# Kernel optimization log

Measured on AMD Instinct MI355X. Metric: run time of the kernel, lower is better.

The kernel has to match this reference:

```python
import jax, jax.numpy as jnp
import numpy as np

V, S, E, H, D, L = 32000, 1024, 512, 8, 64, 4
FF = 4 * E
EPS = 1e-5


def setup_inputs() -> dict:
    key = jax.random.key(0)
    ks = jax.random.split(key, 24)
    s = 0.02
    inp = {
        "x": jax.random.randint(ks[0], (2, S), 0, V, dtype=jnp.int32),
        "tok_emb": jax.random.normal(ks[1], (V, E), jnp.float32) * s,
        "pos_emb": jax.random.normal(ks[2], (S, E), jnp.float32) * s,
        "Wq": jax.random.normal(ks[3], (L, H, E, D), jnp.float32) * s,
        "bq": jnp.zeros((L, H, D), jnp.float32),
        "Wk": jax.random.normal(ks[4], (L, H, E, D), jnp.float32) * s,
        "bk": jnp.zeros((L, H, D), jnp.float32),
        "Wv": jax.random.normal(ks[5], (L, H, E, D), jnp.float32) * s,
        "bv": jnp.zeros((L, H, D), jnp.float32),
        "Wo": jax.random.normal(ks[6], (L, H * D, E), jnp.float32) * s,
        "bo": jnp.zeros((L, E), jnp.float32),
        "W1": jax.random.normal(ks[7], (L, E, FF), jnp.float32) * s,
        "b1": jnp.zeros((L, FF), jnp.float32),
        "W2": jax.random.normal(ks[8], (L, FF, E), jnp.float32) * s,
        "b2": jnp.zeros((L, E), jnp.float32),
        "ln1_g": jnp.ones((L, E), jnp.float32),
        "ln1_b": jnp.zeros((L, E), jnp.float32),
        "ln2_g": jnp.ones((L, E), jnp.float32),
        "ln2_b": jnp.zeros((L, E), jnp.float32),
        "Wout": jax.random.normal(ks[9], (E, V), jnp.float32) * s,
        "bout": jnp.zeros((V,), jnp.float32),
    }
    return inp


def _layernorm(x, g, b):
    mu = jnp.mean(x, axis=-1, keepdims=True)
    var = jnp.mean(jnp.square(x - mu), axis=-1, keepdims=True)
    return (x - mu) * jax.lax.rsqrt(var + EPS) * g + b


def _decoder(h, Wq, bq, Wk, bk, Wv, bv, Wo, bo, W1, b1, W2, b2, g1, be1, g2, be2):
    B, T, _ = h.shape
    # per-head Q/K/V projections, batched over heads (matches concat of per-head linears)
    Q = jnp.einsum("bse,hed->bhsd", h, Wq) + bq[None, :, None, :]
    K = jnp.einsum("bse,hed->bhsd", h, Wk) + bk[None, :, None, :]
    Vv = jnp.einsum("bse,hed->bhsd", h, Wv) + bv[None, :, None, :]
    scores = jnp.einsum("bhqd,bhkd->bhqk", Q, K) / jnp.sqrt(jnp.asarray(D, h.dtype))
    causal = jnp.tril(jnp.ones((T, T), bool))
    scores = jnp.where(causal[None, None], scores, -jnp.inf)
    attn = jax.nn.softmax(scores, axis=-1)
    out = jnp.einsum("bhqk,bhkd->bhqd", attn, Vv)
    conc = out.transpose(0, 2, 1, 3).reshape(B, T, H * D)  # concat heads along feature dim
    mha = conc @ Wo + bo
    ln = _layernorm(h + mha, g1, be1)
    ff = jax.nn.relu(ln @ W1 + b1) @ W2 + b2
    return _layernorm(ln + ff, g2, be2)


def reference(x, tok_emb, pos_emb, Wq, bq, Wk, bk, Wv, bv, Wo, bo,
              W1, b1, W2, b2, ln1_g, ln1_b, ln2_g, ln2_b, Wout, bout):
    B, T = x.shape
    h = tok_emb[x] + pos_emb[:T][None]  # [B,T,E]
    for l in range(L):
        h = _decoder(h, Wq[l], bq[l], Wk[l], bk[l], Wv[l], bv[l], Wo[l], bo[l],
                     W1[l], b1[l], W2[l], b2[l], ln1_g[l], ln1_b[l], ln2_g[l], ln2_b[l])
    return h @ Wout + bout  # [B,T,V] logits
```

## Files before the change

### kernel.cpp

```cpp
#include <hip/hip_runtime.h>
#include <hip/hip_bf16.h>


#define B_ 2
#define S_ 1024
#define E_ 512
#define H_ 8
#define D_ 64
#define L_ 4
#define FF_ 2048
#define V_ 32000
#define M_ (B_ * S_)
#define QKV_N (3 * H_ * D_)

typedef __attribute__((ext_vector_type(8))) short short8;
typedef __attribute__((ext_vector_type(4))) float f32x4;

__device__ __forceinline__ float b2f(ushort u) {
  union { uint32_t i; float f; } c; c.i = ((uint32_t)u) << 16; return c.f;
}
__device__ __forceinline__ ushort f2b(float f) {
  union { float f; uint32_t i; } c; c.f = f;
  uint32_t u = c.i;
  return (ushort)((u + 0x7FFFu + ((u >> 16) & 1u)) >> 16);
}

__device__ __forceinline__ void gload16(const ushort* g, ushort* l) {
  __builtin_amdgcn_global_load_lds(
      (const __attribute__((address_space(1))) void*)g,
      (__attribute__((address_space(3))) void*)l, 16, 0, 0);
}

__global__ __launch_bounds__(256) void embed_kernel(
    const int* __restrict__ x, const float* __restrict__ tok,
    const float* __restrict__ pos, float* __restrict__ hf,
    ushort* __restrict__ hb) {
  int idx = blockIdx.x * 256 + threadIdx.x;
  int e = idx & (E_ - 1);
  int t = (idx >> 9) & (S_ - 1);
  int b = idx >> 19;
  int tokid = x[b * S_ + t];
  float v = tok[(size_t)tokid * E_ + e] + pos[(size_t)t * E_ + e];
  hf[idx] = v;
  hb[idx] = f2b(v);
}

__global__ __launch_bounds__(256) void transpose_cvt_kernel(
    const float* __restrict__ in, ushort* __restrict__ out, int R, int C,
    int B2, long long inS1, long long inS2, long long outS1, long long outS2) {
  __shared__ float tile[32][33];
  int bz = blockIdx.z;
  int b1 = bz / B2, b2 = bz % B2;
  in += (size_t)b1 * inS1 + (size_t)b2 * inS2;
  out += (size_t)b1 * outS1 + (size_t)b2 * outS2;
  int r0 = blockIdx.x * 32, c0 = blockIdx.y * 32;
  int tx = threadIdx.x & 31, ty = threadIdx.x >> 5;
#pragma unroll
  for (int i = 0; i < 4; i++)
    tile[ty + 8 * i][tx] = in[(size_t)(r0 + ty + 8 * i) * C + c0 + tx];
  __syncthreads();
#pragma unroll
  for (int i = 0; i < 4; i++)
    out[(size_t)(c0 + ty + 8 * i) * R + r0 + tx] = f2b(tile[tx][ty + 8 * i]);
}

__global__ __launch_bounds__(256) void qkvw_kernel(
    const float* __restrict__ Wq, const float* __restrict__ Wk,
    const float* __restrict__ Wv, ushort* __restrict__ wqkv) {
  __shared__ float tile[32][33];
  int bz = blockIdx.z;
  int t = bz / (L_ * H_);
  int rem = bz % (L_ * H_);
  int lyr = rem / H_, h = rem % H_;
  const float* in = ((t == 0) ? Wq : (t == 1) ? Wk : Wv) +
                    ((size_t)lyr * H_ + h) * E_ * D_;
  ushort* out = wqkv + (size_t)lyr * QKV_N * E_ + ((size_t)t * 512 + h * 64) * E_;
  int r0 = blockIdx.x * 32, c0 = blockIdx.y * 32;
  int tx = threadIdx.x & 31, ty = threadIdx.x >> 5;
#pragma unroll
  for (int i = 0; i < 4; i++)
    tile[ty + 8 * i][tx] = in[(size_t)(r0 + ty + 8 * i) * D_ + c0 + tx];
  __syncthreads();
#pragma unroll
  for (int i = 0; i < 4; i++)
    out[(size_t)(c0 + ty + 8 * i) * E_ + r0 + tx] = f2b(tile[tx][ty + 8 * i]);
}

__global__ __launch_bounds__(256) void pack_b_kernel(
    const float* __restrict__ bq, const float* __restrict__ bk,
    const float* __restrict__ bv, float* __restrict__ bp) {
  int idx = blockIdx.x * 256 + threadIdx.x;
  if (idx >= L_ * QKV_N) return;
  int n = idx % QKV_N;
  int l = idx / QKV_N;
  int t = n / (H_ * D_);
  int hd = n % (H_ * D_);
  const float* src = (t == 0) ? bq : (t == 1) ? bk : bv;
  bp[idx] = src[(size_t)l * H_ * D_ + hd];
}

template <bool OUTBF, bool RELU, bool VT, bool SWZ>
__global__ __launch_bounds__(256) void mfma_gemm_kernel(
    const ushort* __restrict__ A, const ushort* __restrict__ Bt,
    const float* __restrict__ bias, const float* __restrict__ resid,
    void* __restrict__ out, ushort* __restrict__ vt,
    int M, int N, int K, int gx) {
  __shared__ __align__(16) ushort As[128 * 64];
  __shared__ __align__(16) ushort Bs[128 * 64];
  int tid = threadIdx.x;
  int w = tid >> 6, l = tid & 63;
  int wr = w >> 1, wc = w & 1;
  int lane15 = l & 15, lhi = l >> 4;

  int bid = blockIdx.x;
  int bx, by;
  if (SWZ) {
    int nwg = gx * (M >> 7);
    int wg = (bid & 7) * (nwg >> 3) + (bid >> 3);
    by = wg & ((M >> 7) - 1);
    bx = wg >> 4;
  } else {
    bx = bid % gx;
    by = bid / gx;
  }
  int row0 = by * 128, col0 = bx * 128;

  int rr8 = l >> 3;
  int ksrc = (((l & 7) ^ rr8) << 3);
  const ushort *gA[2][2], *gB[2][2];
  ushort *lA[2][2], *lB[2][2];
#pragma unroll
  for (int cc = 0; cc < 2; cc++) {
    int c = w + cc * 4;
#pragma unroll
    for (int h = 0; h < 2; h++) {
      int row = c * 16 + h * 8 + rr8;
      gA[cc][h] = A + (size_t)(row0 + row) * K + ksrc;
      gB[cc][h] = Bt + (size_t)(col0 + row) * K + ksrc;
      int ldst = c * 1024 + h * 512 + l * 8;
      lA[cc][h] = &As[ldst];
      lB[cc][h] = &Bs[ldst];
    }
  }

  f32x4 acc[4][4] = {};

  for (int k0 = 0; k0 < K; k0 += 64) {
#pragma unroll
    for (int cc = 0; cc < 2; cc++)
#pragma unroll
      for (int h = 0; h < 2; h++) {
        gload16(gA[cc][h] + k0, lA[cc][h]);
        gload16(gB[cc][h] + k0, lB[cc][h]);
      }
    __syncthreads();
    short8 a[4][2], b[4][2];
    int sa = (lane15 & 7) << 4;
#pragma unroll
    for (int i = 0; i < 4; i++) {
      int ra = (wr * 64 + i * 16 + lane15) * 64;
      int rb = (wc * 64 + i * 16 + lane15) * 64;
#pragma unroll
      for (int kk = 0; kk < 2; kk++) {
        int inner = ((kk * 64 + lhi * 16) ^ sa) >> 1;
        a[i][kk] = *(const short8*)&As[ra + inner];
        b[i][kk] = *(const short8*)&Bs[rb + inner];
      }
    }
#pragma unroll
    for (int i = 0; i < 4; i++)
#pragma unroll
      for (int j = 0; j < 4; j++) {
        acc[i][j] = __builtin_amdgcn_mfma_f32_16x16x32_bf16(a[i][0], b[j][0], acc[i][j], 0, 0, 0);
        acc[i][j] = __builtin_amdgcn_mfma_f32_16x16x32_bf16(a[i][1], b[j][1], acc[i][j], 0, 0, 0);
      }
    __syncthreads();
  }

  float* outf = (float*)out;
  ushort* outb = (ushort*)out;
#pragma unroll
  for (int i = 0; i < 4; i++) {
    int gr = row0 + wr * 64 + i * 16 + lhi * 4;
#pragma unroll
    for (int j = 0; j < 4; j++) {
      int gc = col0 + wc * 64 + j * 16 + lane15;
      float bb = bias[gc];
#pragma unroll
      for (int r = 0; r < 4; r++) {
        float v = acc[i][j][r] + bb;
        if (resid) v += resid[(size_t)(gr + r) * N + gc];
        if (RELU) v = fmaxf(v, 0.f);
        if (VT && gc >= 1024) {
          int d = gc - 1024;
          int grr = gr + r;
          int bb2 = grr >> 10, s = grr & 1023;
          vt[(((size_t)(bb2 * 8 + (d >> 6)) * 64 + (d & 63)) << 10) + s] = f2b(v);
        } else if (OUTBF) {
          outb[(size_t)(gr + r) * N + gc] = f2b(v);
        } else {
          outf[(size_t)(gr + r) * N + gc] = v;
        }
      }
    }
  }
}

template <int SK>
__global__ __launch_bounds__(256) void mfma_gemm_sk_kernel(
    const ushort* __restrict__ A, const ushort* __restrict__ Bt,
    float* __restrict__ part, int M, int N, int K, int gx) {
  __shared__ __align__(16) ushort As[128 * 64];
  __shared__ __align__(16) ushort Bs[128 * 64];
  int tid = threadIdx.x;
  int w = tid >> 6, l = tid & 63;
  int wr = w >> 1, wc = w & 1;
  int lane15 = l & 15, lhi = l >> 4;

  int tiles = gx * (M >> 7);
  int sk = blockIdx.x / tiles;
  int rem = blockIdx.x % tiles;
  int bx = rem % gx, by = rem / gx;
  int row0 = by * 128, col0 = bx * 128;
  int klen = K / SK, kbeg = sk * klen;

  int rr8 = l >> 3;
  int ksrc = (((l & 7) ^ rr8) << 3);
  const ushort *gA[2][2], *gB[2][2];
  ushort *lA[2][2], *lB[2][2];
#pragma unroll
  for (int cc = 0; cc < 2; cc++) {
    int c = w + cc * 4;
#pragma unroll
    for (int h = 0; h < 2; h++) {
      int row = c * 16 + h * 8 + rr8;
      gA[cc][h] = A + (size_t)(row0 + row) * K + ksrc;
      gB[cc][h] = Bt + (size_t)(col0 + row) * K + ksrc;
      int ldst = c * 1024 + h * 512 + l * 8;
      lA[cc][h] = &As[ldst];
      lB[cc][h] = &Bs[ldst];
    }
  }

  f32x4 acc[4][4] = {};

  for (int k0 = kbeg; k0 < kbeg + klen; k0 += 64) {
#pragma unroll
    for (int cc = 0; cc < 2; cc++)
#pragma unroll
      for (int h = 0; h < 2; h++) {
        gload16(gA[cc][h] + k0, lA[cc][h]);
        gload16(gB[cc][h] + k0, lB[cc][h]);
      }
    __syncthreads();
    short8 a[4][2], b[4][2];
    int sa = (lane15 & 7) << 4;
#pragma unroll
    for (int i = 0; i < 4; i++) {
      int ra = (wr * 64 + i * 16 + lane15) * 64;
      int rb = (wc * 64 + i * 16 + lane15) * 64;
#pragma unroll
      for (int kk = 0; kk < 2; kk++) {
        int inner = ((kk * 64 + lhi * 16) ^ sa) >> 1;
        a[i][kk] = *(const short8*)&As[ra + inner];
        b[i][kk] = *(const short8*)&Bs[rb + inner];
      }
    }
#pragma unroll
    for (int i = 0; i < 4; i++)
#pragma unroll
      for (int j = 0; j < 4; j++) {
        acc[i][j] = __builtin_amdgcn_mfma_f32_16x16x32_bf16(a[i][0], b[j][0], acc[i][j], 0, 0, 0);
        acc[i][j] = __builtin_amdgcn_mfma_f32_16x16x32_bf16(a[i][1], b[j][1], acc[i][j], 0, 0, 0);
      }
    __syncthreads();
  }

  float* dst = part + (size_t)sk * M * N;
#pragma unroll
  for (int i = 0; i < 4; i++) {
    int gr = row0 + wr * 64 + i * 16 + lhi * 4;
#pragma unroll
    for (int j = 0; j < 4; j++) {
      int gc = col0 + wc * 64 + j * 16 + lane15;
#pragma unroll
      for (int r = 0; r < 4; r++)
        dst[(size_t)(gr + r) * N + gc] = acc[i][j][r];
    }
  }
}

__global__ __launch_bounds__(128) void fattn_kernel(
    const ushort* __restrict__ qkv, const ushort* __restrict__ vt,
    ushort* __restrict__ conc) {
  int qb = blockIdx.x;
  int bh = blockIdx.y;
  int b = bh >> 3, h = bh & 7;
  int w = threadIdx.x >> 6, l = threadIdx.x & 63;
  int lane15 = l & 15, lhi = l >> 4;
  int q0 = qb * 32 + w * 16;

  __shared__ __align__(16) ushort plds[2][16][72];

  const ushort* qr = qkv + (size_t)(b * S_ + q0 + lane15) * QKV_N + h * 64;
  short8 qf0 = *(const short8*)(qr + lhi * 8);
  short8 qf1 = *(const short8*)(qr + 32 + lhi * 8);

  f32x4 o[4] = {};
  float m[4], lsum[4];
#pragma unroll
  for (int r = 0; r < 4; r++) { m[r] = -1e30f; lsum[r] = 0.f; }

  const ushort* kbase = qkv + (size_t)b * S_ * QKV_N + 512 + h * 64;
  const ushort* vbase = vt + (size_t)bh * 64 * S_;
  int qtop = q0 + 15;

  for (int kv0 = 0; kv0 <= qtop; kv0 += 64) {
    float sv[4][4];
#pragma unroll
    for (int t = 0; t < 4; t++) {
      if (kv0 + t * 16 <= qtop) {
        const ushort* kr = kbase + (size_t)(kv0 + t * 16 + lane15) * QKV_N;
        short8 kf0 = *(const short8*)(kr + lhi * 8);
        short8 kf1 = *(const short8*)(kr + 32 + lhi * 8);
        f32x4 s = {};
        s = __builtin_amdgcn_mfma_f32_16x16x32_bf16(qf0, kf0, s, 0, 0, 0);
        s = __builtin_amdgcn_mfma_f32_16x16x32_bf16(qf1, kf1, s, 0, 0, 0);
        int kidx = kv0 + t * 16 + lane15;
#pragma unroll
        for (int r = 0; r < 4; r++) {
          float v = s[r] * 0.125f;
          if (kidx > q0 + lhi * 4 + r) v = -1e30f;
          sv[t][r] = v;
        }
      } else {
#pragma unroll
        for (int r = 0; r < 4; r++) sv[t][r] = -1e30f;
      }
    }
#pragma unroll
    for (int r = 0; r < 4; r++) {
      float rm = fmaxf(fmaxf(sv[0][r], sv[1][r]), fmaxf(sv[2][r], sv[3][r]));
      rm = fmaxf(rm, __shfl_xor(rm, 1));
      rm = fmaxf(rm, __shfl_xor(rm, 2));
      rm = fmaxf(rm, __shfl_xor(rm, 4));
      rm = fmaxf(rm, __shfl_xor(rm, 8));
      float mn = fmaxf(m[r], rm);
      float sc = __expf(m[r] - mn);
      m[r] = mn;
      float rs = 0.f;
#pragma unroll
      for (int t = 0; t < 4; t++) {
        float p = __expf(sv[t][r] - mn);
        plds[w][lhi * 4 + r][t * 16 + lane15] = f2b(p);
        rs += p;
      }
      rs += __shfl_xor(rs, 1);
      rs += __shfl_xor(rs, 2);
      rs += __shfl_xor(rs, 4);
      rs += __shfl_xor(rs, 8);
      lsum[r] = lsum[r] * sc + rs;
#pragma unroll
      for (int n = 0; n < 4; n++) o[n][r] *= sc;
    }
    short8 pa0 = *(const short8*)&plds[w][lane15][lhi * 8];
    short8 pa1 = *(const short8*)&plds[w][lane15][32 + lhi * 8];
#pragma unroll
    for (int n = 0; n < 4; n++) {
      const ushort* vr = vbase + (size_t)(n * 16 + lane15) * S_ + kv0;
      short8 vf0 = *(const short8*)(vr + lhi * 8);
      short8 vf1 = *(const short8*)(vr + 32 + lhi * 8);
      o[n] = __builtin_amdgcn_mfma_f32_16x16x32_bf16(pa0, vf0, o[n], 0, 0, 0);
      o[n] = __builtin_amdgcn_mfma_f32_16x16x32_bf16(pa1, vf1, o[n], 0, 0, 0);
    }
  }
#pragma unroll
  for (int r = 0; r < 4; r++) {
    float inv = 1.f / lsum[r];
    int row = b * S_ + q0 + lhi * 4 + r;
#pragma unroll
    for (int n = 0; n < 4; n++)
      conc[(size_t)row * (H_ * D_) + h * 64 + n * 16 + lane15] = f2b(o[n][r] * inv);
  }
}

template <int SK>
__global__ __launch_bounds__(256) void ln_red_kernel(
    const float* __restrict__ part, const float* __restrict__ bias,
    const float* __restrict__ resid, const float* __restrict__ g,
    const float* __restrict__ bsh, float* __restrict__ outf,
    ushort* __restrict__ outb) {
  int w = threadIdx.x >> 6, l = threadIdx.x & 63;
  int row = blockIdx.x * 4 + w;
  size_t off = (size_t)row * E_ + l * 8;
  float4 r0 = *(const float4*)(resid + off);
  float4 r1 = *(const float4*)(resid + off + 4);
  float4 bb0 = *(const float4*)(bias + l * 8);
  float4 bb1 = *(const float4*)(bias + l * 8 + 4);
  float x[8] = {r0.x + bb0.x, r0.y + bb0.y, r0.z + bb0.z, r0.w + bb0.w,
                r1.x + bb1.x, r1.y + bb1.y, r1.z + bb1.z, r1.w + bb1.w};
#pragma unroll
  for (int s = 0; s < SK; s++) {
    const float* ps = part + (size_t)s * M_ * E_ + off;
    float4 p0 = *(const float4*)ps;
    float4 p1 = *(const float4*)(ps + 4);
    x[0] += p0.x; x[1] += p0.y; x[2] += p0.z; x[3] += p0.w;
    x[4] += p1.x; x[5] += p1.y; x[6] += p1.z; x[7] += p1.w;
  }
  float s = 0.f, q = 0.f;
#pragma unroll
  for (int i = 0; i < 8; i++) { s += x[i]; q += x[i] * x[i]; }
#pragma unroll
  for (int off2 = 1; off2 < 64; off2 <<= 1) {
    s += __shfl_xor(s, off2);
    q += __shfl_xor(q, off2);
  }
  float mu = s * (1.f / 512.f);
  float var = q * (1.f / 512.f) - mu * mu;
  float rs = rsqrtf(var + 1e-5f);
  float4 g0 = *(const float4*)(g + l * 8);
  float4 g1 = *(const float4*)(g + l * 8 + 4);
  float4 b0 = *(const float4*)(bsh + l * 8);
  float4 b1 = *(const float4*)(bsh + l * 8 + 4);
  float gg[8] = {g0.x, g0.y, g0.z, g0.w, g1.x, g1.y, g1.z, g1.w};
  float bbv[8] = {b0.x, b0.y, b0.z, b0.w, b1.x, b1.y, b1.z, b1.w};
  float y[8];
#pragma unroll
  for (int i = 0; i < 8; i++) y[i] = (x[i] - mu) * rs * gg[i] + bbv[i];
  float* of = outf + off;
  *(float4*)of = make_float4(y[0], y[1], y[2], y[3]);
  *(float4*)(of + 4) = make_float4(y[4], y[5], y[6], y[7]);
  ushort4 u0 = {f2b(y[0]), f2b(y[1]), f2b(y[2]), f2b(y[3])};
  ushort4 u1 = {f2b(y[4]), f2b(y[5]), f2b(y[6]), f2b(y[7])};
  ushort* ob = outb + off;
  *(ushort4*)ob = u0;
  *(ushort4*)(ob + 4) = u1;
}

extern "C" void kernel_launch(void* const* d_in, const int* in_sizes, int n_in,
                              void* d_out, int out_size, void* d_ws, size_t ws_size,
                              hipStream_t stream) {
  const int* x = (const int*)d_in[0];
  const float* tok = (const float*)d_in[1];
  const float* pos = (const float*)d_in[2];
  const float* Wq = (const float*)d_in[3];
  const float* bq = (const float*)d_in[4];
  const float* Wk = (const float*)d_in[5];
  const float* bk = (const float*)d_in[6];
  const float* Wv = (const float*)d_in[7];
  const float* bv = (const float*)d_in[8];
  const float* Wo = (const float*)d_in[9];
  const float* bo = (const float*)d_in[10];
  const float* W1 = (const float*)d_in[11];
  const float* b1 = (const float*)d_in[12];
  const float* W2 = (const float*)d_in[13];
  const float* b2 = (const float*)d_in[14];
  const float* ln1g = (const float*)d_in[15];
  const float* ln1b = (const float*)d_in[16];
  const float* ln2g = (const float*)d_in[17];
  const float* ln2b = (const float*)d_in[18];
  const float* Wout = (const float*)d_in[19];
  const float* bout = (const float*)d_in[20];
  float* out = (float*)d_out;

  char* p = (char*)d_ws;
  auto alloc = [&](size_t bytes) {
    char* r = p;
    p += (bytes + 255) & ~(size_t)255;
    return r;
  };
  float* h_f = (float*)alloc((size_t)M_ * E_ * 4);
  ushort* h_b = (ushort*)alloc((size_t)M_ * E_ * 2);
  ushort* qkv_b = (ushort*)alloc((size_t)M_ * QKV_N * 2);
  ushort* conc_b = (ushort*)alloc((size_t)M_ * E_ * 2);
  float* part = (float*)alloc((size_t)4 * M_ * E_ * 4);
  float* ln_f = (float*)alloc((size_t)M_ * E_ * 4);
  ushort* ln_b = (ushort*)alloc((size_t)M_ * E_ * 2);
  ushort* ff_b = (ushort*)alloc((size_t)M_ * FF_ * 2);
  ushort* vt_b = (ushort*)alloc((size_t)B_ * H_ * D_ * S_ * 2);
  ushort* wqkv = (ushort*)alloc((size_t)L_ * QKV_N * E_ * 2);
  float* bqkv = (float*)alloc((size_t)L_ * QKV_N * 4);
  ushort* wo_t = (ushort*)alloc((size_t)L_ * E_ * E_ * 2);
  ushort* w1_t = (ushort*)alloc((size_t)L_ * FF_ * E_ * 2);
  ushort* w2_t = (ushort*)alloc((size_t)L_ * E_ * FF_ * 2);
  ushort* wout_t = (ushort*)alloc((size_t)V_ * E_ * 2);

  qkvw_kernel<<<dim3(E_ / 32, D_ / 32, 3 * L_ * H_), 256, 0, stream>>>(Wq, Wk, Wv, wqkv);
  transpose_cvt_kernel<<<dim3(16, 16, L_), 256, 0, stream>>>(
      Wo, wo_t, 512, 512, 1, (long long)512 * 512, 0, (long long)512 * 512, 0);
  transpose_cvt_kernel<<<dim3(E_ / 32, FF_ / 32, L_), 256, 0, stream>>>(
      W1, w1_t, E_, FF_, 1, (long long)E_ * FF_, 0, (long long)FF_ * E_, 0);
  transpose_cvt_kernel<<<dim3(FF_ / 32, E_ / 32, L_), 256, 0, stream>>>(
      W2, w2_t, FF_, E_, 1, (long long)FF_ * E_, 0, (long long)E_ * FF_, 0);
  transpose_cvt_kernel<<<dim3(E_ / 32, V_ / 32, 1), 256, 0, stream>>>(
      Wout, wout_t, E_, V_, 1, 0, 0, 0, 0);
  pack_b_kernel<<<(L_ * QKV_N + 255) / 256, 256, 0, stream>>>(bq, bk, bv, bqkv);

  embed_kernel<<<(M_ * E_) / 256, 256, 0, stream>>>(x, tok, pos, h_f, h_b);

  for (int l = 0; l < L_; ++l) {
    mfma_gemm_kernel<true, false, true, false><<<(QKV_N / 128) * (M_ / 128), 256, 0, stream>>>(
        h_b, wqkv + (size_t)l * QKV_N * E_, bqkv + l * QKV_N, nullptr,
        qkv_b, vt_b, M_, QKV_N, E_, QKV_N / 128);
    fattn_kernel<<<dim3(S_ / 32, B_ * H_), 128, 0, stream>>>(qkv_b, vt_b, conc_b);
    mfma_gemm_sk_kernel<4><<<4 * (E_ / 128) * (M_ / 128), 256, 0, stream>>>(
        conc_b, wo_t + (size_t)l * E_ * E_, part, M_, E_, E_, E_ / 128);
    ln_red_kernel<4><<<M_ / 4, 256, 0, stream>>>(
        part, bo + l * E_, h_f, ln1g + l * E_, ln1b + l * E_, ln_f, ln_b);
    mfma_gemm_kernel<true, true, false, false><<<(FF_ / 128) * (M_ / 128), 256, 0, stream>>>(
        ln_b, w1_t + (size_t)l * FF_ * E_, b1 + l * FF_, nullptr, ff_b, nullptr,
        M_, FF_, E_, FF_ / 128);
    mfma_gemm_sk_kernel<4><<<4 * (E_ / 128) * (M_ / 128), 256, 0, stream>>>(
        ff_b, w2_t + (size_t)l * E_ * FF_, part, M_, E_, FF_, E_ / 128);
    ln_red_kernel<4><<<M_ / 4, 256, 0, stream>>>(
        part, b2 + l * E_, ln_f, ln2g + l * E_, ln2b + l * E_, h_f, h_b);
  }

  mfma_gemm_kernel<false, false, false, true><<<(V_ / 128) * (M_ / 128), 256, 0, stream>>>(
      h_b, wout_t, bout, nullptr, out, nullptr, M_, V_, E_, V_ / 128);
}
```

Baseline: 660.2 us.

## Use 256x256-tile double-buffered GEMM kernel for output vocab projection

Replaces the 128x128 swizzled GEMM for the final logits projection with a new 512-thread kernel that computes 256x256 output tiles and double-buffers its LDS stages so the next K slice loads while the current one is computed. Larger tiles halve the operand reloads per output element for this large fp32-output GEMM, and the block ordering is swizzled by XCD. The cost is 128 KB of LDS and heavy register use per block, which limits occupancy, and the launch count (1000 blocks) is hardcoded.

```diff
diff --git a/kernel.cpp b/kernel.cpp
--- a/kernel.cpp
+++ b/kernel.cpp
@@ -99,7 +99,7 @@
   bp[idx] = src[(size_t)l * H_ * D_ + hd];
 }
 
-template <bool OUTBF, bool RELU, bool VT, bool SWZ>
+template <bool OUTBF, bool RELU, bool VT>
 __global__ __launch_bounds__(256) void mfma_gemm_kernel(
     const ushort* __restrict__ A, const ushort* __restrict__ Bt,
     const float* __restrict__ bias, const float* __restrict__ resid,
@@ -113,16 +113,7 @@
   int lane15 = l & 15, lhi = l >> 4;
 
   int bid = blockIdx.x;
-  int bx, by;
-  if (SWZ) {
-    int nwg = gx * (M >> 7);
-    int wg = (bid & 7) * (nwg >> 3) + (bid >> 3);
-    by = wg & ((M >> 7) - 1);
-    bx = wg >> 4;
-  } else {
-    bx = bid % gx;
-    by = bid / gx;
-  }
+  int bx = bid % gx, by = bid / gx;
   int row0 = by * 128, col0 = bx * 128;
 
   int rr8 = l >> 3;
@@ -286,6 +277,94 @@
 #pragma unroll
       for (int r = 0; r < 4; r++)
         dst[(size_t)(gr + r) * N + gc] = acc[i][j][r];
+    }
+  }
+}
+
+__global__ __launch_bounds__(512) void mfma_gemm256_kernel(
+    const ushort* __restrict__ A, const ushort* __restrict__ Bt,
+    const float* __restrict__ bias, float* __restrict__ out,
+    int M, int N, int K) {
+  __shared__ __align__(16) ushort As[2][256 * 64];
+  __shared__ __align__(16) ushort Bs[2][256 * 64];
+  int tid = threadIdx.x;
+  int w = tid >> 6, l = tid & 63;
+  int wr = w >> 2, wc = w & 3;
+  int lane15 = l & 15, lhi = l >> 4;
+
+  int bid = blockIdx.x;
+  int wg = (bid & 7) * 125 + (bid >> 3);
+  int by = wg & 7, bx = wg >> 3;
+  int row0 = by * 256, col0 = bx * 256;
+
+  const ushort* ga[4];
+  const ushort* gb[4];
+  int lofs[4];
+#pragma unroll
+  for (int p2 = 0; p2 < 4; p2++) {
+    int i = p2 * 512 + tid;
+    int row = i >> 3, kg = i & 7;
+    int ksrc = ((kg ^ (row & 7)) << 3);
+    ga[p2] = A + (size_t)(row0 + row) * K + ksrc;
+    gb[p2] = Bt + (size_t)(col0 + row) * K + ksrc;
+    lofs[p2] = i * 8;
+  }
+
+  f32x4 acc[8][4] = {};
+
+  auto stage = [&](int buf, int k0) {
+    ushort* bA = &As[buf][0];
+    ushort* bB = &Bs[buf][0];
+#pragma unroll
+    for (int p2 = 0; p2 < 4; p2++) {
+      gload16(ga[p2] + k0, bA + lofs[p2]);
+      gload16(gb[p2] + k0, bB + lofs[p2]);
+    }
+  };
+  auto compute = [&](int buf) {
+    const ushort* bA = &As[buf][0];
+    const ushort* bB = &Bs[buf][0];
+    int sa = (lane15 & 7) << 4;
+#pragma unroll
+    for (int kk = 0; kk < 2; kk++) {
+      int inner = ((kk * 64 + lhi * 16) ^ sa) >> 1;
+      short8 a[8], b[4];
+#pragma unroll
+      for (int i = 0; i < 8; i++)
+        a[i] = *(const short8*)&bA[(wr * 128 + i * 16 + lane15) * 64 + inner];
+#pragma unroll
+      for (int j = 0; j < 4; j++)
+        b[j] = *(const short8*)&bB[(wc * 64 + j * 16 + lane15) * 64 + inner];
+#pragma unroll
+      for (int i = 0; i < 8; i++)
+#pragma unroll
+        for (int j = 0; j < 4; j++)
+          acc[i][j] = __builtin_amdgcn_mfma_f32_16x16x32_bf16(a[i], b[j], acc[i][j], 0, 0, 0);
+    }
+  };
+
+  stage(0, 0);
+  __syncthreads();
+  int cur = 0;
+  int nt = K >> 6;
+  for (int t = 0; t < nt - 1; t++) {
+    stage(cur ^ 1, (t + 1) << 6);
+    compute(cur);
+    __syncthreads();
+    cur ^= 1;
+  }
+  compute(cur);
+
+#pragma unroll
+  for (int i = 0; i < 8; i++) {
+    int gr = row0 + wr * 128 + i * 16 + lhi * 4;
+#pragma unroll
+    for (int j = 0; j < 4; j++) {
+      int gc = col0 + wc * 64 + j * 16 + lane15;
+      float bb = bias[gc];
+#pragma unroll
+      for (int r = 0; r < 4; r++)
+        out[(size_t)(gr + r) * N + gc] = acc[i][j][r] + bb;
     }
   }
 }
@@ -499,7 +578,7 @@
   embed_kernel<<<(M_ * E_) / 256, 256, 0, stream>>>(x, tok, pos, h_f, h_b);
 
   for (int l = 0; l < L_; ++l) {
-    mfma_gemm_kernel<true, false, true, false><<<(QKV_N / 128) * (M_ / 128), 256, 0, stream>>>(
+    mfma_gemm_kernel<true, false, true><<<(QKV_N / 128) * (M_ / 128), 256, 0, stream>>>(
         h_b, wqkv + (size_t)l * QKV_N * E_, bqkv + l * QKV_N, nullptr,
         qkv_b, vt_b, M_, QKV_N, E_, QKV_N / 128);
     fattn_kernel<<<dim3(S_ / 32, B_ * H_), 128, 0, stream>>>(qkv_b, vt_b, conc_b);
@@ -507,7 +586,7 @@
         conc_b, wo_t + (size_t)l * E_ * E_, part, M_, E_, E_, E_ / 128);
     ln_red_kernel<4><<<M_ / 4, 256, 0, stream>>>(
         part, bo + l * E_, h_f, ln1g + l * E_, ln1b + l * E_, ln_f, ln_b);
-    mfma_gemm_kernel<true, true, false, false><<<(FF_ / 128) * (M_ / 128), 256, 0, stream>>>(
+    mfma_gemm_kernel<true, true, false><<<(FF_ / 128) * (M_ / 128), 256, 0, stream>>>(
         ln_b, w1_t + (size_t)l * FF_ * E_, b1 + l * FF_, nullptr, ff_b, nullptr,
         M_, FF_, E_, FF_ / 128);
     mfma_gemm_sk_kernel<4><<<4 * (E_ / 128) * (M_ / 128), 256, 0, stream>>>(
@@ -516,6 +595,6 @@
         part, b2 + l * E_, ln_f, ln2g + l * E_, ln2b + l * E_, h_f, h_b);
   }
 
-  mfma_gemm_kernel<false, false, false, true><<<(V_ / 128) * (M_ / 128), 256, 0, stream>>>(
-      h_b, wout_t, bout, nullptr, out, nullptr, M_, V_, E_, V_ / 128);
-}
+  mfma_gemm256_kernel<<<(M_ / 256) * (V_ / 256), 512, 0, stream>>>(
+      h_b, wout_t, bout, out, M_, V_, E_);
+}
```

Result: no change. 651.9 us (-1.3%).
